# Kernel optimization log

Hardware: AMD Instinct MI355X
Metric: run time of the kernel (lower is better)

Reference implementation:

```python
import jax, jax.numpy as jnp
import numpy as np

NUM_CLASSES = 9
TEMP = 0.1
ALPHA = 0.99
EPS = 1e-12  # F.normalize default eps


def _l2norm(x, axis=-1):
    n = jnp.linalg.norm(x, axis=axis, keepdims=True)
    return x / jnp.maximum(n, EPS)


def setup_inputs() -> dict:
    key = jax.random.key(0)
    k1, k2, k3, k4, k5 = jax.random.split(key, 5)
    B, D, h, w = 4, 768, 128, 128
    return {
        "cls_score": jax.random.normal(k1, (B, NUM_CLASSES, h, w), dtype=jnp.float32),
        "label": jax.random.randint(k2, (B, 4 * h, 4 * w), 0, NUM_CLASSES, dtype=jnp.int64),
        "gt_lucas": jax.random.randint(k3, (B, 4 * h, 4 * w), 0, NUM_CLASSES, dtype=jnp.int64),
        "features": jax.random.normal(k4, (B, D, h, w), dtype=jnp.float32),
        "prototypes": jax.random.uniform(k5, (NUM_CLASSES, D), dtype=jnp.float32),
    }


def reference(cls_score, label, gt_lucas, features, prototypes):
    B, D, h, w = features.shape
    # so the masked gathers reduce to a full flatten (static shapes).
    corine = label[:, ::4, ::4].reshape(-1)          # [N]
    lucas = gt_lucas[:, ::4, ::4].reshape(-1)        # [N] (mask trivially all valid)
    feats = jnp.transpose(features, (0, 2, 3, 1)).reshape(-1, D)  # [N, D]
    N = feats.shape[0]
    # note: original indexes corine labels under the lucas mask (mask all-true here)
    labels_lucas = corine
    labels_corine = jnp.where(corine == 7, 6, corine)
    # per-class EMA prototype update (unique(labels_lucas) == arange(9) by construction;
    # compute_ema detaches the new mean)
    sums = jax.ops.segment_sum(feats, labels_lucas, num_segments=NUM_CLASSES)      # [C, D]
    counts = jax.ops.segment_sum(jnp.ones((N,), feats.dtype), labels_lucas,
                                 num_segments=NUM_CLASSES)                          # [C]
    means = jax.lax.stop_gradient(sums / counts[:, None])
    protos = ALPHA * means + (1.0 - ALPHA) * prototypes
    protos = _l2norm(protos, axis=-1)                # F.normalize over feature dim
    logits = protos @ feats.T                        # [C, N]
    prot_feat = _l2norm(logits, axis=-1) / TEMP      # normalize each class row over N
    prot_feat = prot_feat.at[2].set((labels_corine == 2).astype(prot_feat.dtype))
    E = jnp.exp(prot_feat)                           # [C, N]
    A1 = E[labels_corine, jnp.arange(N)]             # [N]
    A2 = E.sum(axis=0)                               # [N]
    return jnp.mean(-jnp.log(A1 / A2))
```

## Files before the change

### kernel.cpp

```cpp
#include <hip/hip_runtime.h>
#include <math.h>

#define NCLS 9
#define DIM 768
#define NPIX 65536

#define OFF_LAB     ((size_t)0)
#define OFF_HIST    ((size_t)262144)
#define OFF_SUMS    ((size_t)271360)
#define OFF_SUMSQ   ((size_t)299008)
#define OFF_LOSS    ((size_t)299072)
#define OFF_DONE    ((size_t)299088)
#define OFF_PROTO   ((size_t)299136)
#define OFF_LOGITS  ((size_t)336128)
#define OFF_PART    ((size_t)2695424)

__device__ __forceinline__ float waveReduceSum(float v) {
#pragma unroll
  for (int off = 32; off > 0; off >>= 1) v += __shfl_down(v, off, 64);
  return v;
}

__global__ void k0_lab(const int* __restrict__ label, int* __restrict__ lab,
                       int* __restrict__ hist) {
  __shared__ int h[NCLS];
  int tid = threadIdx.x;
  if (tid < NCLS) h[tid] = 0;
  __syncthreads();
  int n = blockIdx.x * 256 + tid;
  int b = n >> 14, r = (n >> 7) & 127, cc = n & 127;
  int c = label[b * 262144 + r * 2048 + cc * 4];
  lab[n] = c;
  atomicAdd(&h[c], 1);
  __syncthreads();
  if (tid < NCLS) hist[blockIdx.x * NCLS + tid] = h[tid];
}

__global__ void k1_segsum(const float4* __restrict__ feat4, const int4* __restrict__ lab4,
                          float* __restrict__ sums) {
  int d = blockIdx.x;
  int tid = threadIdx.x;
  float acc[NCLS];
#pragma unroll
  for (int k = 0; k < NCLS; ++k) acc[k] = 0.f;
  for (int b = 0; b < 4; ++b) {
    const float4* fp = feat4 + (size_t)(b * DIM + d) * 4096;
    const int4* lp = lab4 + b * 4096;
    for (int p = tid; p < 4096; p += 256) {
      float4 f = fp[p];
      int4 l = lp[p];
#pragma unroll
      for (int k = 0; k < NCLS; ++k) {
        acc[k] += (l.x == k) ? f.x : 0.f;
        acc[k] += (l.y == k) ? f.y : 0.f;
        acc[k] += (l.z == k) ? f.z : 0.f;
        acc[k] += (l.w == k) ? f.w : 0.f;
      }
    }
  }
  __shared__ float red[4][NCLS];
#pragma unroll
  for (int k = 0; k < NCLS; ++k) acc[k] = waveReduceSum(acc[k]);
  int lane = tid & 63, w = tid >> 6;
  if (lane == 0) {
#pragma unroll
    for (int k = 0; k < NCLS; ++k) red[w][k] = acc[k];
  }
  __syncthreads();
  if (tid < NCLS)
    sums[tid * DIM + d] = red[0][tid] + red[1][tid] + red[2][tid] + red[3][tid];
}

__global__ void k2_proto(const float* __restrict__ sums, const int* __restrict__ hist,
                         const float* __restrict__ proto, float* __restrict__ protoT,
                         float* __restrict__ sumsq, float* __restrict__ lossacc,
                         unsigned int* __restrict__ done) {
  __shared__ float red[12][NCLS];
  __shared__ float inv[NCLS];
  __shared__ float cpart[16][NCLS];
  __shared__ float cnt[NCLS];
  int tid = threadIdx.x;
  if (tid < 144) {
    int c = tid % NCLS, g = tid / NCLS;
    int s = 0;
#pragma unroll
    for (int j = 0; j < 16; ++j) s += hist[(g * 16 + j) * NCLS + c];
    cpart[g][c] = (float)s;
  }
  if (tid >= 192 && tid < 208) sumsq[tid - 192] = 0.f;
  if (tid == 208) lossacc[0] = 0.f;
  if (tid == 209) done[0] = 0u;
  __syncthreads();
  if (tid < NCLS) {
    float s = 0.f;
#pragma unroll
    for (int g = 0; g < 16; ++g) s += cpart[g][tid];
    cnt[tid] = s;
  }
  __syncthreads();
  float v[NCLS];
#pragma unroll
  for (int c = 0; c < NCLS; ++c)
    v[c] = 0.99f * (sums[c * DIM + tid] / cnt[c]) + 0.01f * proto[c * DIM + tid];
  int lane = tid & 63, w = tid >> 6;
#pragma unroll
  for (int c = 0; c < NCLS; ++c) {
    float q = waveReduceSum(v[c] * v[c]);
    if (lane == 0) red[w][c] = q;
  }
  __syncthreads();
  if (tid < NCLS) {
    float t = 0.f;
#pragma unroll
    for (int w2 = 0; w2 < 12; ++w2) t += red[w2][tid];
    inv[tid] = 1.f / fmaxf(sqrtf(t), 1e-12f);
  }
  __syncthreads();
#pragma unroll
  for (int c = 0; c < NCLS; ++c) protoT[tid * 12 + c] = v[c] * inv[c];
}

__global__ void k3_logits(const float* __restrict__ feat, const float* __restrict__ protoT,
                          float* __restrict__ part) {
  __shared__ float pl[192 * 12];
  int tid = threadIdx.x;
  int s = blockIdx.x & 3;
  int chunk = blockIdx.x >> 2;
  const float* src = protoT + (size_t)s * 192 * 12;
  for (int i = tid; i < 192 * 12; i += 256) pl[i] = src[i];
  __syncthreads();
  int n = chunk * 256 + tid;
  int b = n >> 14, p = n & 16383;
  const float* fp = feat + ((size_t)(b * DIM + s * 192)) * 16384 + p;
  float a0 = 0, a1 = 0, a2 = 0, a3 = 0, a4 = 0, a5 = 0, a6 = 0, a7 = 0, a8 = 0;
#pragma unroll 4
  for (int dd = 0; dd < 192; ++dd) {
    float f = fp[(size_t)dd * 16384];
    const float4* pr = (const float4*)&pl[dd * 12];
    float4 q0 = pr[0];
    float4 q1 = pr[1];
    float q8 = pl[dd * 12 + 8];
    a0 += q0.x * f; a1 += q0.y * f; a2 += q0.z * f; a3 += q0.w * f;
    a4 += q1.x * f; a5 += q1.y * f; a6 += q1.z * f; a7 += q1.w * f;
    a8 += q8 * f;
  }
  float* out = part + ((size_t)s * NCLS) * NPIX + n;
  out[0 * NPIX] = a0; out[1 * NPIX] = a1; out[2 * NPIX] = a2;
  out[3 * NPIX] = a3; out[4 * NPIX] = a4; out[5 * NPIX] = a5;
  out[6 * NPIX] = a6; out[7 * NPIX] = a7; out[8 * NPIX] = a8;
}

__global__ void k4_combine(const float4* __restrict__ part4, float4* __restrict__ logits4,
                           float* __restrict__ sumsq) {
  int t = blockIdx.x * 256 + threadIdx.x;
  int tid = threadIdx.x;
  float ssq[NCLS];
#pragma unroll
  for (int c = 0; c < NCLS; ++c) {
    float4 v = part4[(size_t)(0 * NCLS + c) * 16384 + t];
#pragma unroll
    for (int s = 1; s < 4; ++s) {
      float4 wv = part4[(size_t)(s * NCLS + c) * 16384 + t];
      v.x += wv.x; v.y += wv.y; v.z += wv.z; v.w += wv.w;
    }
    logits4[(size_t)c * 16384 + t] = v;
    ssq[c] = v.x * v.x + v.y * v.y + v.z * v.z + v.w * v.w;
  }
  __shared__ float red[4][NCLS];
#pragma unroll
  for (int c = 0; c < NCLS; ++c) ssq[c] = waveReduceSum(ssq[c]);
  int lane = tid & 63, w = tid >> 6;
  if (lane == 0) {
#pragma unroll
    for (int c = 0; c < NCLS; ++c) red[w][c] = ssq[c];
  }
  __syncthreads();
  if (tid < NCLS)
    atomicAdd(&sumsq[tid], red[0][tid] + red[1][tid] + red[2][tid] + red[3][tid]);
}

__global__ void k5_loss(const float4* __restrict__ logits4, const int4* __restrict__ lab4,
                        const float* __restrict__ sumsq, float* __restrict__ lossacc,
                        unsigned int* __restrict__ done, float* __restrict__ out) {
  int t = blockIdx.x * 256 + threadIdx.x;
  int tid = threadIdx.x;
  float scale[NCLS];
#pragma unroll
  for (int c = 0; c < NCLS; ++c) scale[c] = 10.f / fmaxf(sqrtf(sumsq[c]), 1e-12f);
  float arr[NCLS][4];
#pragma unroll
  for (int c = 0; c < NCLS; ++c) {
    float4 v = logits4[(size_t)c * 16384 + t];
    arr[c][0] = v.x; arr[c][1] = v.y; arr[c][2] = v.z; arr[c][3] = v.w;
  }
  int4 lb = lab4[t];
  int lv[4] = {lb.x, lb.y, lb.z, lb.w};
  float lsum = 0.f;
#pragma unroll
  for (int j = 0; j < 4; ++j) {
    int l = lv[j];
    int lc = (l == 7) ? 6 : l;
    float sumE = 0.f, picked = 0.f;
#pragma unroll
    for (int c = 0; c < NCLS; ++c) {
      float pf = (c == 2) ? ((lc == 2) ? 1.f : 0.f) : arr[c][j] * scale[c];
      sumE += __expf(pf);
      picked += (c == lc) ? pf : 0.f;
    }
    lsum += __logf(sumE) - picked;
  }
  lsum = waveReduceSum(lsum);
  __shared__ float red[4];
  int lane = tid & 63, w = tid >> 6;
  if (lane == 0) red[w] = lsum;
  __syncthreads();
  if (tid == 0) {
    atomicAdd(lossacc, red[0] + red[1] + red[2] + red[3]);
    __threadfence();
    unsigned int ticket = atomicAdd(done, 1u);
    if (ticket == gridDim.x - 1) {
      __threadfence();
      float total = __hip_atomic_load(lossacc, __ATOMIC_ACQUIRE, __HIP_MEMORY_SCOPE_AGENT);
      out[0] = total * (1.f / (float)NPIX);
    }
  }
}

extern "C" void kernel_launch(void* const* d_in, const int* in_sizes, int n_in,
                              void* d_out, int out_size, void* d_ws, size_t ws_size,
                              hipStream_t stream) {
  const int* label = (const int*)d_in[1];
  const float* feat = (const float*)d_in[3];
  const float* proto = (const float*)d_in[4];
  char* ws = (char*)d_ws;
  int* lab = (int*)(ws + OFF_LAB);
  int* hist = (int*)(ws + OFF_HIST);
  float* sums = (float*)(ws + OFF_SUMS);
  float* sumsq = (float*)(ws + OFF_SUMSQ);
  float* lossacc = (float*)(ws + OFF_LOSS);
  unsigned int* done = (unsigned int*)(ws + OFF_DONE);
  float* protoT = (float*)(ws + OFF_PROTO);
  float* logits = (float*)(ws + OFF_LOGITS);
  float* part = (float*)(ws + OFF_PART);

  k0_lab<<<NPIX / 256, 256, 0, stream>>>(label, lab, hist);
  k1_segsum<<<DIM, 256, 0, stream>>>((const float4*)feat, (const int4*)lab, sums);
  k2_proto<<<1, 768, 0, stream>>>(sums, hist, proto, protoT, sumsq, lossacc, done);
  k3_logits<<<(NPIX / 256) * 4, 256, 0, stream>>>(feat, protoT, part);
  k4_combine<<<64, 256, 0, stream>>>((const float4*)part, (float4*)logits, sumsq);
  k5_loss<<<64, 256, 0, stream>>>((const float4*)logits, (const int4*)lab, sumsq, lossacc, done,
                                  (float*)d_out);
}
```

Measured before the change: 104.4 us.

## Fuse proto normalization, logits and combine into one kernel; byte labels

Merges the single-block prototype kernel, the split-K logits kernel and the combine kernel into one 1024-thread kernel. Each block recomputes the normalized prototypes in shared memory and reduces the four D-slices through LDS, so the partial-logits buffer round trip and two launches go away. Labels are stored as bytes to shrink label traffic, and the accumulator reset moves into the first kernel. The cost is that every one of 256 blocks redundantly reads sums, proto and hist, and each block now needs about 37KB of LDS, which may limit occupancy.

Result: faster. 98.60 us (-5.5%).

```diff
diff --git a/kernel.cpp b/kernel.cpp
--- a/kernel.cpp
+++ b/kernel.cpp
@@ -6,14 +6,12 @@
 #define NPIX 65536
 
 #define OFF_LAB     ((size_t)0)
-#define OFF_HIST    ((size_t)262144)
-#define OFF_SUMS    ((size_t)271360)
-#define OFF_SUMSQ   ((size_t)299008)
-#define OFF_LOSS    ((size_t)299072)
-#define OFF_DONE    ((size_t)299088)
-#define OFF_PROTO   ((size_t)299136)
-#define OFF_LOGITS  ((size_t)336128)
-#define OFF_PART    ((size_t)2695424)
+#define OFF_HIST    ((size_t)65536)
+#define OFF_SUMS    ((size_t)74752)
+#define OFF_SUMSQ   ((size_t)102400)
+#define OFF_LOSS    ((size_t)102464)
+#define OFF_DONE    ((size_t)102480)
+#define OFF_LOGITS  ((size_t)131072)
 
 __device__ __forceinline__ float waveReduceSum(float v) {
 #pragma unroll
@@ -21,8 +19,9 @@
   return v;
 }
 
-__global__ void k0_lab(const int* __restrict__ label, int* __restrict__ lab,
-                       int* __restrict__ hist) {
+__global__ void k0_lab(const int* __restrict__ label, unsigned char* __restrict__ lab,
+                       int* __restrict__ hist, float* __restrict__ sumsq,
+                       float* __restrict__ lossacc, unsigned int* __restrict__ done) {
   __shared__ int h[NCLS];
   int tid = threadIdx.x;
   if (tid < NCLS) h[tid] = 0;
@@ -30,13 +29,18 @@
   int n = blockIdx.x * 256 + tid;
   int b = n >> 14, r = (n >> 7) & 127, cc = n & 127;
   int c = label[b * 262144 + r * 2048 + cc * 4];
-  lab[n] = c;
+  lab[n] = (unsigned char)c;
   atomicAdd(&h[c], 1);
+  if (blockIdx.x == 0) {
+    if (tid < 16) sumsq[tid] = 0.f;
+    else if (tid == 16) lossacc[0] = 0.f;
+    else if (tid == 17) done[0] = 0u;
+  }
   __syncthreads();
   if (tid < NCLS) hist[blockIdx.x * NCLS + tid] = h[tid];
 }
 
-__global__ void k1_segsum(const float4* __restrict__ feat4, const int4* __restrict__ lab4,
+__global__ void k1_segsum(const float4* __restrict__ feat4, const uchar4* __restrict__ lab4,
                           float* __restrict__ sums) {
   int d = blockIdx.x;
   int tid = threadIdx.x;
@@ -45,16 +49,19 @@
   for (int k = 0; k < NCLS; ++k) acc[k] = 0.f;
   for (int b = 0; b < 4; ++b) {
     const float4* fp = feat4 + (size_t)(b * DIM + d) * 4096;
-    const int4* lp = lab4 + b * 4096;
-    for (int p = tid; p < 4096; p += 256) {
+    const uchar4* lp = lab4 + b * 4096;
+#pragma unroll 4
+    for (int i = 0; i < 16; ++i) {
+      int p = tid + i * 256;
       float4 f = fp[p];
-      int4 l = lp[p];
+      uchar4 l = lp[p];
+      int lx = l.x, ly = l.y, lz = l.z, lw = l.w;
 #pragma unroll
       for (int k = 0; k < NCLS; ++k) {
-        acc[k] += (l.x == k) ? f.x : 0.f;
-        acc[k] += (l.y == k) ? f.y : 0.f;
-        acc[k] += (l.z == k) ? f.z : 0.f;
-        acc[k] += (l.w == k) ? f.w : 0.f;
+        acc[k] += (lx == k) ? f.x : 0.f;
+        acc[k] += (ly == k) ? f.y : 0.f;
+        acc[k] += (lz == k) ? f.z : 0.f;
+        acc[k] += (lw == k) ? f.w : 0.f;
       }
     }
   }
@@ -71,115 +78,113 @@
     sums[tid * DIM + d] = red[0][tid] + red[1][tid] + red[2][tid] + red[3][tid];
 }
 
-__global__ void k2_proto(const float* __restrict__ sums, const int* __restrict__ hist,
-                         const float* __restrict__ proto, float* __restrict__ protoT,
-                         float* __restrict__ sumsq, float* __restrict__ lossacc,
-                         unsigned int* __restrict__ done) {
-  __shared__ float red[12][NCLS];
-  __shared__ float inv[NCLS];
-  __shared__ float cpart[16][NCLS];
+__global__ void __launch_bounds__(1024) k3_fused(const float* __restrict__ sums,
+                                                 const int* __restrict__ hist,
+                                                 const float* __restrict__ proto,
+                                                 const float* __restrict__ feat,
+                                                 float* __restrict__ logits,
+                                                 float* __restrict__ sumsq) {
+  __shared__ float pl[DIM * 12];
+  __shared__ float cpart[32][NCLS];
   __shared__ float cnt[NCLS];
-  int tid = threadIdx.x;
-  if (tid < 144) {
+  __shared__ float red12[12][NCLS];
+  __shared__ float invn[NCLS];
+  __shared__ float red4[4][NCLS];
+  int tid = threadIdx.x;
+
+  if (tid < 288) {
     int c = tid % NCLS, g = tid / NCLS;
     int s = 0;
 #pragma unroll
-    for (int j = 0; j < 16; ++j) s += hist[(g * 16 + j) * NCLS + c];
+    for (int j = 0; j < 8; ++j) s += hist[(g * 8 + j) * NCLS + c];
     cpart[g][c] = (float)s;
   }
-  if (tid >= 192 && tid < 208) sumsq[tid - 192] = 0.f;
-  if (tid == 208) lossacc[0] = 0.f;
-  if (tid == 209) done[0] = 0u;
   __syncthreads();
   if (tid < NCLS) {
     float s = 0.f;
 #pragma unroll
-    for (int g = 0; g < 16; ++g) s += cpart[g][tid];
+    for (int g = 0; g < 32; ++g) s += cpart[g][tid];
     cnt[tid] = s;
   }
   __syncthreads();
+
   float v[NCLS];
-#pragma unroll
-  for (int c = 0; c < NCLS; ++c)
-    v[c] = 0.99f * (sums[c * DIM + tid] / cnt[c]) + 0.01f * proto[c * DIM + tid];
-  int lane = tid & 63, w = tid >> 6;
-#pragma unroll
-  for (int c = 0; c < NCLS; ++c) {
-    float q = waveReduceSum(v[c] * v[c]);
-    if (lane == 0) red[w][c] = q;
+  if (tid < DIM) {
+#pragma unroll
+    for (int c = 0; c < NCLS; ++c)
+      v[c] = 0.99f * (sums[c * DIM + tid] / cnt[c]) + 0.01f * proto[c * DIM + tid];
+    int lane = tid & 63, w = tid >> 6;
+#pragma unroll
+    for (int c = 0; c < NCLS; ++c) {
+      float q = waveReduceSum(v[c] * v[c]);
+      if (lane == 0) red12[w][c] = q;
+    }
   }
   __syncthreads();
   if (tid < NCLS) {
     float t = 0.f;
 #pragma unroll
-    for (int w2 = 0; w2 < 12; ++w2) t += red[w2][tid];
-    inv[tid] = 1.f / fmaxf(sqrtf(t), 1e-12f);
-  }
-  __syncthreads();
-#pragma unroll
-  for (int c = 0; c < NCLS; ++c) protoT[tid * 12 + c] = v[c] * inv[c];
-}
-
-__global__ void k3_logits(const float* __restrict__ feat, const float* __restrict__ protoT,
-                          float* __restrict__ part) {
-  __shared__ float pl[192 * 12];
-  int tid = threadIdx.x;
-  int s = blockIdx.x & 3;
-  int chunk = blockIdx.x >> 2;
-  const float* src = protoT + (size_t)s * 192 * 12;
-  for (int i = tid; i < 192 * 12; i += 256) pl[i] = src[i];
-  __syncthreads();
-  int n = chunk * 256 + tid;
-  int b = n >> 14, p = n & 16383;
-  const float* fp = feat + ((size_t)(b * DIM + s * 192)) * 16384 + p;
+    for (int w2 = 0; w2 < 12; ++w2) t += red12[w2][tid];
+    invn[tid] = 1.f / fmaxf(sqrtf(t), 1e-12f);
+  }
+  __syncthreads();
+  if (tid < DIM) {
+#pragma unroll
+    for (int c = 0; c < NCLS; ++c) pl[tid * 12 + c] = v[c] * invn[c];
+  }
+  __syncthreads();
+
+  int s = tid >> 8, p = tid & 255;
+  int n = blockIdx.x * 256 + p;
+  int b = n >> 14, pp = n & 16383;
+  const float* fp = feat + ((size_t)(b * DIM + s * 192)) * 16384 + pp;
+  const float* plbase = pl + (size_t)s * 192 * 12;
   float a0 = 0, a1 = 0, a2 = 0, a3 = 0, a4 = 0, a5 = 0, a6 = 0, a7 = 0, a8 = 0;
 #pragma unroll 4
   for (int dd = 0; dd < 192; ++dd) {
     float f = fp[(size_t)dd * 16384];
-    const float4* pr = (const float4*)&pl[dd * 12];
+    const float4* pr = (const float4*)(plbase + dd * 12);
     float4 q0 = pr[0];
     float4 q1 = pr[1];
-    float q8 = pl[dd * 12 + 8];
+    float q8 = plbase[dd * 12 + 8];
     a0 += q0.x * f; a1 += q0.y * f; a2 += q0.z * f; a3 += q0.w * f;
     a4 += q1.x * f; a5 += q1.y * f; a6 += q1.z * f; a7 += q1.w * f;
     a8 += q8 * f;
   }
-  float* out = part + ((size_t)s * NCLS) * NPIX + n;
-  out[0 * NPIX] = a0; out[1 * NPIX] = a1; out[2 * NPIX] = a2;
-  out[3 * NPIX] = a3; out[4 * NPIX] = a4; out[5 * NPIX] = a5;
-  out[6 * NPIX] = a6; out[7 * NPIX] = a7; out[8 * NPIX] = a8;
-}
-
-__global__ void k4_combine(const float4* __restrict__ part4, float4* __restrict__ logits4,
-                           float* __restrict__ sumsq) {
-  int t = blockIdx.x * 256 + threadIdx.x;
-  int tid = threadIdx.x;
-  float ssq[NCLS];
-#pragma unroll
-  for (int c = 0; c < NCLS; ++c) {
-    float4 v = part4[(size_t)(0 * NCLS + c) * 16384 + t];
-#pragma unroll
-    for (int s = 1; s < 4; ++s) {
-      float4 wv = part4[(size_t)(s * NCLS + c) * 16384 + t];
-      v.x += wv.x; v.y += wv.y; v.z += wv.z; v.w += wv.w;
-    }
-    logits4[(size_t)c * 16384 + t] = v;
-    ssq[c] = v.x * v.x + v.y * v.y + v.z * v.z + v.w * v.w;
-  }
-  __shared__ float red[4][NCLS];
-#pragma unroll
-  for (int c = 0; c < NCLS; ++c) ssq[c] = waveReduceSum(ssq[c]);
-  int lane = tid & 63, w = tid >> 6;
-  if (lane == 0) {
-#pragma unroll
-    for (int c = 0; c < NCLS; ++c) red[w][c] = ssq[c];
+  __syncthreads();
+  if (s > 0) {
+    float* rp = pl + (size_t)(s - 1) * 2304 + p * 9;
+    rp[0] = a0; rp[1] = a1; rp[2] = a2; rp[3] = a3; rp[4] = a4;
+    rp[5] = a5; rp[6] = a6; rp[7] = a7; rp[8] = a8;
+  }
+  __syncthreads();
+  if (s == 0) {
+#pragma unroll
+    for (int q = 0; q < 3; ++q) {
+      const float* rp = pl + (size_t)q * 2304 + p * 9;
+      a0 += rp[0]; a1 += rp[1]; a2 += rp[2]; a3 += rp[3]; a4 += rp[4];
+      a5 += rp[5]; a6 += rp[6]; a7 += rp[7]; a8 += rp[8];
+    }
+    float* outp = logits + n;
+    outp[0 * NPIX] = a0; outp[1 * NPIX] = a1; outp[2 * NPIX] = a2;
+    outp[3 * NPIX] = a3; outp[4 * NPIX] = a4; outp[5 * NPIX] = a5;
+    outp[6 * NPIX] = a6; outp[7 * NPIX] = a7; outp[8 * NPIX] = a8;
+    float ss[NCLS] = {a0 * a0, a1 * a1, a2 * a2, a3 * a3, a4 * a4,
+                      a5 * a5, a6 * a6, a7 * a7, a8 * a8};
+#pragma unroll
+    for (int c = 0; c < NCLS; ++c) ss[c] = waveReduceSum(ss[c]);
+    int lane = tid & 63, w = tid >> 6;
+    if (lane == 0) {
+#pragma unroll
+      for (int c = 0; c < NCLS; ++c) red4[w][c] = ss[c];
+    }
   }
   __syncthreads();
   if (tid < NCLS)
-    atomicAdd(&sumsq[tid], red[0][tid] + red[1][tid] + red[2][tid] + red[3][tid]);
-}
-
-__global__ void k5_loss(const float4* __restrict__ logits4, const int4* __restrict__ lab4,
+    atomicAdd(&sumsq[tid], red4[0][tid] + red4[1][tid] + red4[2][tid] + red4[3][tid]);
+}
+
+__global__ void k5_loss(const float4* __restrict__ logits4, const uchar4* __restrict__ lab4,
                         const float* __restrict__ sumsq, float* __restrict__ lossacc,
                         unsigned int* __restrict__ done, float* __restrict__ out) {
   int t = blockIdx.x * 256 + threadIdx.x;
@@ -193,7 +198,7 @@
     float4 v = logits4[(size_t)c * 16384 + t];
     arr[c][0] = v.x; arr[c][1] = v.y; arr[c][2] = v.z; arr[c][3] = v.w;
   }
-  int4 lb = lab4[t];
+  uchar4 lb = lab4[t];
   int lv[4] = {lb.x, lb.y, lb.z, lb.w};
   float lsum = 0.f;
 #pragma unroll
@@ -233,21 +238,17 @@
   const float* feat = (const float*)d_in[3];
   const float* proto = (const float*)d_in[4];
   char* ws = (char*)d_ws;
-  int* lab = (int*)(ws + OFF_LAB);
+  unsigned char* lab = (unsigned char*)(ws + OFF_LAB);
   int* hist = (int*)(ws + OFF_HIST);
   float* sums = (float*)(ws + OFF_SUMS);
   float* sumsq = (float*)(ws + OFF_SUMSQ);
   float* lossacc = (float*)(ws + OFF_LOSS);
   unsigned int* done = (unsigned int*)(ws + OFF_DONE);
-  float* protoT = (float*)(ws + OFF_PROTO);
   float* logits = (float*)(ws + OFF_LOGITS);
-  float* part = (float*)(ws + OFF_PART);
-
-  k0_lab<<<NPIX / 256, 256, 0, stream>>>(label, lab, hist);
-  k1_segsum<<<DIM, 256, 0, stream>>>((const float4*)feat, (const int4*)lab, sums);
-  k2_proto<<<1, 768, 0, stream>>>(sums, hist, proto, protoT, sumsq, lossacc, done);
-  k3_logits<<<(NPIX / 256) * 4, 256, 0, stream>>>(feat, protoT, part);
-  k4_combine<<<64, 256, 0, stream>>>((const float4*)part, (float4*)logits, sumsq);
-  k5_loss<<<64, 256, 0, stream>>>((const float4*)logits, (const int4*)lab, sumsq, lossacc, done,
-                                  (float*)d_out);
-}
+
+  k0_lab<<<NPIX / 256, 256, 0, stream>>>(label, lab, hist, sumsq, lossacc, done);
+  k1_segsum<<<DIM, 256, 0, stream>>>((const float4*)feat, (const uchar4*)lab, sums);
+  k3_fused<<<NPIX / 256, 1024, 0, stream>>>(sums, hist, proto, feat, logits, sumsq);
+  k5_loss<<<64, 256, 0, stream>>>((const float4*)logits, (const uchar4*)lab, sumsq, lossacc,
+                                  done, (float*)d_out);
+}
```
